# Performance work log

Measured on AMD Instinct MI355X. Metric: run time of the kernel, lower is better.

Reference implementation:

```python
import jax, jax.numpy as jnp
import numpy as np

T, B, D, H = 2048, 2, 1024, 16
DPH = D // H
SCALE = DPH ** -0.5


def setup_inputs() -> dict:
    key = jax.random.key(0)
    ks = jax.random.split(key, 5)
    x = jax.random.normal(ks[0], (T, B, D), dtype=jnp.float32)
    Wk = jax.random.normal(ks[1], (D, D), dtype=jnp.float32) * 0.02
    Wv = jax.random.normal(ks[2], (D, D), dtype=jnp.float32) * 0.02
    Wq = jax.random.normal(ks[3], (D, D), dtype=jnp.float32) * 0.02
    Wo = jax.random.normal(ks[4], (D, D), dtype=jnp.float32) * 0.02
    # causal mask: True marks positions to hide (masked_fill semantics)
    mask = jnp.triu(jnp.ones((T, T), dtype=bool), k=1)
    return {"x": x, "Wk": Wk, "Wv": Wv, "Wq": Wq, "Wo": Wo, "mask": mask}


def _split_heads(y):
    # 't b (d h) -> b h t d' : d_per_head is the OUTER factor of the split
    t, b, _ = y.shape
    return y.reshape(t, b, DPH, H).transpose(1, 3, 0, 2)  # [b, h, t, d]


def reference(x, Wk, Wv, Wq, Wo, mask):
    # nn.Linear(bias=False): y = x @ W.T
    k = _split_heads(x @ Wk.T)
    v = _split_heads(x @ Wv.T)
    q = _split_heads(x @ Wq.T)
    scores = jnp.einsum('bhid,bhjd->bhij', q, k) * SCALE  # [b,h,t,t]
    scores = jnp.where(mask, -jnp.inf, scores)
    attn = jax.nn.softmax(scores, axis=-1)
    # dropout is identity in eval mode
    out = jnp.einsum('bhij,bhjd->bhid', attn, v)  # [b,h,t,d]
    # 'b h t d -> t b (h d)' : heads are the OUTER factor of the merge
    out = out.transpose(2, 0, 1, 3).reshape(x.shape[0], x.shape[1], D)
    return out @ Wo.T
```

## Files before the change

kernel.cpp:

```cpp
#include <hip/hip_runtime.h>

#define T_LEN   2048
#define BATCH   2
#define DMODEL  1024
#define NHEAD   16
#define DHEAD   64
#define MROWS   4096
#define KDIM    1024
#define NDIM    1024
#define ATT_SC2 (0.125f * 1.44269504088896f)

typedef unsigned short u16;
typedef unsigned int   u32;
typedef u16   u16x8 __attribute__((ext_vector_type(8)));
typedef u16   u16x4 __attribute__((ext_vector_type(4)));
typedef __bf16 bf16x8 __attribute__((ext_vector_type(8)));
typedef float f32x4 __attribute__((ext_vector_type(4)));

__device__ __forceinline__ u16 f2bf(float f) {
  u32 u = __builtin_bit_cast(u32, f);
  u += 0x7fffu + ((u >> 16) & 1u);
  return (u16)(u >> 16);
}

__device__ __forceinline__ u16 bfc(float f) {
  return __builtin_bit_cast(u16, (__bf16)f);
}

__device__ __forceinline__ f32x4 mfma16(u16x8 a, u16x8 b, f32x4 c) {
  return __builtin_amdgcn_mfma_f32_16x16x32_bf16(
      __builtin_bit_cast(bf16x8, a), __builtin_bit_cast(bf16x8, b), c, 0, 0, 0);
}

__device__ __forceinline__ void gload16(const u16* g, u16* l) {
  __builtin_amdgcn_global_load_lds((const __attribute__((address_space(1))) void*)g,
                                   (__attribute__((address_space(3))) void*)l,
                                   16, 0, 0);
}

#define XN 4194304u
__global__ __launch_bounds__(256) void cast_all(
    const float* __restrict__ x,  const float* __restrict__ wk,
    const float* __restrict__ wv, const float* __restrict__ wq,
    const float* __restrict__ wo, u16* __restrict__ ws) {
  size_t i = ((size_t)blockIdx.x * 256 + threadIdx.x) * 4;
  const float* src; size_t soff, doff; float sc = 1.0f;
  if (i < XN) {
    int m = (int)(i >> 10), d = (int)(i & 1023);
    int t = m >> 1, b = m & 1;
    src = x; soff = i;
    doff = ((size_t)(b * 2048 + t) << 10) + d;
  } else {
    size_t off = i - XN;
    int wi = (int)(off >> 20);
    off &= 1048575u;
    int u = (int)(off >> 10), c = (int)(off & 1023);
    src = (wi == 0) ? wk : (wi == 1) ? wv : (wi == 2) ? wq : wo;
    soff = off;
    if (wi == 3) {
      doff = XN + 3u * 1048576u + off;
    } else {
      int slot = (wi == 2) ? 0 : (wi == 0) ? 1 : 2;
      int up = (u & 15) * 64 + (u >> 4);
      doff = XN + (size_t)slot * 1048576u + ((size_t)up << 10) + c;
      if (wi == 2) sc = ATT_SC2;
    }
  }
  float4 v = *reinterpret_cast<const float4*>(src + soff);
  u16x4 o;
  o.s0 = f2bf(v.x * sc); o.s1 = f2bf(v.y * sc); o.s2 = f2bf(v.z * sc); o.s3 = f2bf(v.w * sc);
  *reinterpret_cast<u16x4*>(ws + doff) = o;
}

__global__ __launch_bounds__(256, 2) void gemm_qkv(
    const u16* __restrict__ xbm, const u16* __restrict__ Wqkv,
    u16* __restrict__ Qh, u16* __restrict__ Kh, u16* __restrict__ Vt) {
  __shared__ __align__(16) u16 As[256 * 64];
  __shared__ __align__(16) u16 Bs[128 * 64];

  const int tid = threadIdx.x;
  const int l  = tid & 63, w = tid >> 6;
  const int lr = l & 15,  lg = l >> 4;
  const int wm = w >> 1,  wn = w & 1;

  const int blk  = blockIdx.x;
  const int wgid = (blk & 7) * 48 + (blk >> 3);

  const u16 *A, *W;
  int m0, n0, isV;
  if (wgid < 256) {
    const int bx = wgid >> 4, by = wgid & 15;
    A = xbm; W = Wqkv; m0 = by * 256; n0 = bx * 128; isV = 0;
  } else {
    const int v = wgid - 256;
    const int vby = v >> 5, vbx = v & 31;
    A = Wqkv + (2048u << 10); W = xbm; m0 = vby * 256; n0 = vbx * 128; isV = 1;
  }

  f32x4 acc[8][4];
#pragma unroll
  for (int i = 0; i < 8; ++i)
#pragma unroll
    for (int j = 0; j < 4; ++j) acc[i][j] = (f32x4)(0.0f);

  for (int k0 = 0; k0 < KDIM; k0 += 64) {
#pragma unroll
    for (int i = 0; i < 8; ++i) {
      const int base = i * 256 + w * 64;
      const int p = base + l;
      const int r = p >> 3, c = p & 7;
      gload16(A + (size_t)(m0 + r) * KDIM + k0 + ((c ^ (r & 7)) << 3),
              As + (size_t)base * 8);
    }
#pragma unroll
    for (int i = 0; i < 4; ++i) {
      const int base = i * 256 + w * 64;
      const int p = base + l;
      const int r = p >> 3, c = p & 7;
      gload16(W + (size_t)(n0 + r) * KDIM + k0 + ((c ^ (r & 7)) << 3),
              Bs + (size_t)base * 8);
    }
    __syncthreads();

#pragma unroll
    for (int ks = 0; ks < 2; ++ks) {
      const int cr = ks * 4 + lg;
      u16x8 bf_[4];
#pragma unroll
      for (int ni = 0; ni < 4; ++ni) {
        const int rr = wn * 64 + ni * 16 + lr;
        bf_[ni] = *reinterpret_cast<const u16x8*>(Bs + rr * 64 + ((cr ^ (rr & 7)) << 3));
      }
      __builtin_amdgcn_s_setprio(1);
#pragma unroll
      for (int mi = 0; mi < 8; ++mi) {
        const int rr = wm * 128 + mi * 16 + lr;
        const u16x8 af = *reinterpret_cast<const u16x8*>(
            As + rr * 64 + ((cr ^ (rr & 7)) << 3));
#pragma unroll
        for (int ni = 0; ni < 4; ++ni)
          acc[mi][ni] = mfma16(af, bf_[ni], acc[mi][ni]);
      }
      __builtin_amdgcn_s_setprio(0);
    }
    __syncthreads();
  }

#pragma unroll
  for (int mi = 0; mi < 8; ++mi)
#pragma unroll
    for (int ni = 0; ni < 4; ++ni)
#pragma unroll
      for (int r = 0; r < 4; ++r) {
        const int row = m0 + wm * 128 + mi * 16 + lg * 4 + r;
        const int col = n0 + wn * 64 + ni * 16 + lr;
        const u16 v = bfc(acc[mi][ni][r]);
        if (!isV) {
          const int bb = row >> 11, t = row & 2047;
          const int c = col & 1023, hh = c >> 6, dp = c & 63;
          u16* d = (col < 1024) ? Qh : Kh;
          d[(((size_t)(bb * NHEAD + hh) << 11) + t) * 64 + dp] = v;
        } else {
          const int hh = row >> 6, dp = row & 63;
          const int bb = col >> 11, t = col & 2047;
          Vt[((((size_t)(bb * NHEAD + hh)) * 64 + dp) << 11) + t] = v;
        }
      }
}

__global__ __launch_bounds__(256) void gemm_o(
    const u16* __restrict__ A, const u16* __restrict__ W, float* __restrict__ out) {
  __shared__ __align__(16) u16 As[128 * 64];
  __shared__ __align__(16) u16 Bs[64 * 64];

  const int tid = threadIdx.x;
  const int l  = tid & 63, w = tid >> 6;
  const int lr = l & 15,  lg = l >> 4;
  const int wm = w >> 1,  wn = w & 1;

  const int blk  = blockIdx.x;
  const int wgid = (blk & 7) * 64 + (blk >> 3);
  const int bx = wgid >> 5, by = wgid & 31;
  const int m0 = by * 128;
  const int n0 = bx * 64;

  f32x4 acc[4][2];
#pragma unroll
  for (int i = 0; i < 4; ++i)
#pragma unroll
    for (int j = 0; j < 2; ++j) acc[i][j] = (f32x4)(0.0f);

  for (int k0 = 0; k0 < KDIM; k0 += 64) {
#pragma unroll
    for (int i = 0; i < 4; ++i) {
      const int base = i * 256 + w * 64;
      const int p = base + l;
      const int r = p >> 3, c = p & 7;
      gload16(A + (size_t)(m0 + r) * KDIM + k0 + ((c ^ (r & 7)) << 3),
              As + (size_t)base * 8);
    }
#pragma unroll
    for (int i = 0; i < 2; ++i) {
      const int base = i * 256 + w * 64;
      const int p = base + l;
      const int r = p >> 3, c = p & 7;
      gload16(W + (size_t)(n0 + r) * KDIM + k0 + ((c ^ (r & 7)) << 3),
              Bs + (size_t)base * 8);
    }
    __syncthreads();

#pragma unroll
    for (int ks = 0; ks < 2; ++ks) {
      const int cr = ks * 4 + lg;
      u16x8 bf_[2];
#pragma unroll
      for (int ni = 0; ni < 2; ++ni) {
        const int rr = wn * 32 + ni * 16 + lr;
        bf_[ni] = *reinterpret_cast<const u16x8*>(Bs + rr * 64 + ((cr ^ (rr & 7)) << 3));
      }
      __builtin_amdgcn_s_setprio(1);
#pragma unroll
      for (int mi = 0; mi < 4; ++mi) {
        const int rr = wm * 64 + mi * 16 + lr;
        const u16x8 af = *reinterpret_cast<const u16x8*>(
            As + rr * 64 + ((cr ^ (rr & 7)) << 3));
#pragma unroll
        for (int ni = 0; ni < 2; ++ni)
          acc[mi][ni] = mfma16(af, bf_[ni], acc[mi][ni]);
      }
      __builtin_amdgcn_s_setprio(0);
    }
    __syncthreads();
  }

#pragma unroll
  for (int mi = 0; mi < 4; ++mi)
#pragma unroll
    for (int ni = 0; ni < 2; ++ni)
#pragma unroll
      for (int r = 0; r < 4; ++r) {
        const int row = m0 + wm * 64 + mi * 16 + lg * 4 + r;
        const int col = n0 + wn * 32 + ni * 16 + lr;
        const int t = row & 2047, bb = row >> 11;
        out[((size_t)(t * 2 + bb) << 10) + col] = acc[mi][ni][r];
      }
}

__global__ __launch_bounds__(256, 2) void attn_fwd(
    const u16* __restrict__ Qh, const u16* __restrict__ Kh,
    const u16* __restrict__ Vt, u16* __restrict__ Aout) {
  __shared__ __align__(16) u16 smem[36864];

  const int tid = threadIdx.x;
  const int l = tid & 63, w = tid >> 6;
  const int lr = l & 15, lg = l >> 4;
  const int wk = w & 1, wq = w >> 1;
  const int blk = blockIdx.x;
  const int bxx = (blk >> 3) & 15;
  const int bh  = ((blk >> 7) << 3) + (blk & 7);
  const int b = bh >> 4, h = bh & 15;

  const u16* kg = Kh + ((size_t)bh << 17);
  const u16* vg = Vt + ((size_t)bh << 17);
  u16* Pw = smem + 32768 + w * 1024;

  float* redO = reinterpret_cast<float*>(smem);
  float* redS = reinterpret_cast<float*>(smem + 32768);

  const u16x8 ones = {0x3F80,0x3F80,0x3F80,0x3F80,0x3F80,0x3F80,0x3F80,0x3F80};

  auto stage = [&](int buf, int kv0) {
    u16* kb = smem + buf * 8192;
    u16* vb = smem + 16384 + buf * 8192;
#pragma unroll
    for (int j = 0; j < 4; ++j) {
      const int base = (j * 4 + w) * 64;
      const int gg = base + l;
      const int rk = gg >> 3, ck = gg & 7;
      gload16(kg + (size_t)(kv0 + rk) * 64 + ((ck ^ (rk & 7)) << 3),
              kb + (size_t)base * 8);
      const int rv = gg >> 4, cv = gg & 15;
      gload16(vg + ((size_t)rv << 11) + kv0 + ((cv ^ (rv & 15)) << 3),
              vb + (size_t)base * 8);
    }
  };

  for (int ph = 0; ph < 2; ++ph) {
    const int qb = ph ? bxx : 31 - bxx;
    const int qbw = qb * 64 + wq * 32;

    u16x8 qf[2][2];
#pragma unroll
    for (int g = 0; g < 2; ++g) {
      const int qrow = qbw + g * 16 + lr;
      const u16* qptr = Qh + (((size_t)bh << 11) + qrow) * 64 + lg * 8;
      qf[g][0] = *reinterpret_cast<const u16x8*>(qptr);
      qf[g][1] = *reinterpret_cast<const u16x8*>(qptr + 32);
    }

    f32x4 oacc[2][4];
#pragma unroll
    for (int g = 0; g < 2; ++g)
#pragma unroll
      for (int i = 0; i < 4; ++i) oacc[g][i] = (f32x4)(0.0f);
    f32x4 sum4[2] = {(f32x4)(0.0f), (f32x4)(0.0f)};

    const int npair = (qb + 2) >> 1;
    stage(0, 0);
    __syncthreads();

    int cur = 0;
    for (int t = 0; t < npair; ++t) {
      const int kv0 = t * 128;
      if (t + 1 < npair) stage(cur ^ 1, kv0 + 128);

      const int kvw = kv0 + wk * 64;
      if (kvw <= qbw + 31) {
        const u16* kb = smem + cur * 8192;
        const u16* vb = smem + 16384 + cur * 8192;

        u16x8 kf[4][2];
#pragma unroll
        for (int tt = 0; tt < 4; ++tt) {
          const int row = wk * 64 + tt * 16 + lr;
          kf[tt][0] = *reinterpret_cast<const u16x8*>(
              kb + row * 64 + ((lg ^ (row & 7)) << 3));
          kf[tt][1] = *reinterpret_cast<const u16x8*>(
              kb + row * 64 + (((4 + lg) ^ (row & 7)) << 3));
        }
        u16x8 vf[2][4];
#pragma unroll
        for (int kh = 0; kh < 2; ++kh)
#pragma unroll
          for (int ni = 0; ni < 4; ++ni) {
            const int dr = ni * 16 + lr;
            const int ck = wk * 8 + kh * 4 + lg;
            vf[kh][ni] = *reinterpret_cast<const u16x8*>(
                vb + dr * 128 + ((ck ^ (dr & 15)) << 3));
          }

#pragma unroll
        for (int g = 0; g < 2; ++g) {
          const int qbg = qbw + g * 16;
          if (kvw <= qbg + 15) {
            const bool diag = (kvw + 63 > qbg);
            const int qrow = qbg + lr;

            __builtin_amdgcn_s_setprio(1);
#pragma unroll
            for (int tt = 0; tt < 4; ++tt) {
              f32x4 sacc = (f32x4)(0.0f);
              sacc = mfma16(kf[tt][0], qf[g][0], sacc);
              sacc = mfma16(kf[tt][1], qf[g][1], sacc);
              u16x4 pk;
#pragma unroll
              for (int r = 0; r < 4; ++r) {
                const int kv = kvw + tt * 16 + lg * 4 + r;
                const float s = (diag && kv > qrow) ? -1e30f : sacc[r];
                pk[r] = bfc(__builtin_amdgcn_exp2f(s - 8.0f));
              }
              *reinterpret_cast<u16x4*>(
                  &Pw[lr * 64 + (((tt * 2 + (lg >> 1)) ^ (lr & 7)) << 3)
                      + ((lg & 1) << 2)]) = pk;
            }

#pragma unroll
            for (int kh = 0; kh < 2; ++kh) {
              const u16x8 pa = *reinterpret_cast<const u16x8*>(
                  &Pw[lr * 64 + (((kh * 4 + lg) ^ (lr & 7)) << 3)]);
              sum4[g] = mfma16(pa, ones, sum4[g]);
#pragma unroll
              for (int ni = 0; ni < 4; ++ni)
                oacc[g][ni] = mfma16(pa, vf[kh][ni], oacc[g][ni]);
            }
            __builtin_amdgcn_s_setprio(0);
          }
        }
      }

      __syncthreads();
      cur ^= 1;
    }

    if (wk) {
      float* po = redO + wq * 2176;
#pragma unroll
      for (int g = 0; g < 2; ++g) {
#pragma unroll
        for (int ni = 0; ni < 4; ++ni)
#pragma unroll
          for (int r = 0; r < 4; ++r)
            po[(g * 16 + lg * 4 + r) * 68 + ni * 16 + lr] = oacc[g][ni][r];
        if (lr == 0) {
#pragma unroll
          for (int r = 0; r < 4; ++r)
            redS[wq * 32 + g * 16 + lg * 4 + r] = sum4[g][r];
        }
      }
    }
    __syncthreads();

    if (!wk) {
      const float* po = redO + wq * 2176;
#pragma unroll
      for (int g = 0; g < 2; ++g) {
        f32x4 ss = sum4[g];
#pragma unroll
        for (int r = 0; r < 4; ++r)
          ss[r] += redS[wq * 32 + g * 16 + lg * 4 + r];
#pragma unroll
        for (int r = 0; r < 4; ++r) {
          const float inv = 1.0f / ss[r];
          const int q = qbw + g * 16 + lg * 4 + r;
          const size_t rowbase = (((size_t)(b * 2048 + q)) << 10) + h * DHEAD;
#pragma unroll
          for (int ni = 0; ni < 4; ++ni)
            Aout[rowbase + ni * 16 + lr] = bfc(
                (oacc[g][ni][r] + po[(g * 16 + lg * 4 + r) * 68 + ni * 16 + lr])
                * inv);
        }
      }
    }
    __syncthreads();
  }
}

extern "C" void kernel_launch(void* const* d_in, const int* in_sizes, int n_in,
                              void* d_out, int out_size, void* d_ws, size_t ws_size,
                              hipStream_t stream) {
  const float* x  = (const float*)d_in[0];
  const float* Wk = (const float*)d_in[1];
  const float* Wv = (const float*)d_in[2];
  const float* Wq = (const float*)d_in[3];
  const float* Wo = (const float*)d_in[4];

  u16* ws   = (u16*)d_ws;
  u16* xbm  = ws;
  u16* Wqkv = xbm + 4194304;
  u16* Wob  = Wqkv + 3145728;
  u16* Qh   = Wob + 1048576;
  u16* Kh   = Qh  + 4194304;
  u16* Vt   = Kh  + 4194304;
  u16* Aout = Vt  + 4194304;

  cast_all<<<8192, 256, 0, stream>>>(x, Wk, Wv, Wq, Wo, ws);

  gemm_qkv<<<384, 256, 0, stream>>>(xbm, Wqkv, Qh, Kh, Vt);

  attn_fwd<<<512, 256, 0, stream>>>(Qh, Kh, Vt, Aout);

  gemm_o<<<512, 256, 0, stream>>>(Aout, Wob, (float*)d_out);
}
```

Measured before the change: 107.1 us.

## Process both causal-balanced query blocks in one shared KV sweep

The attention kernel previously handled two query blocks (31-bxx and bxx) one after another, streaming K/V tiles from global memory twice. It now loads Q fragments for both blocks up front and makes a single pass over the KV range of the longer block, applying each staged K/V tile to both query blocks. This removes the duplicate K/V staging and one set of pipeline start-ups and barriers. The cost is twice the accumulator and Q registers per thread, which under launch_bounds(256,2) may cause spills or lower occupancy, and the reduction area in shared memory doubles.

After: 110.1 us. 2.8% more time.

```diff
diff --git a/kernel.cpp b/kernel.cpp
--- a/kernel.cpp
+++ b/kernel.cpp
@@ -260,6 +260,8 @@
   const int bh  = ((blk >> 7) << 3) + (blk & 7);
   const int b = bh >> 4, h = bh & 15;
 
+  const int qb_[2] = {31 - bxx, bxx};
+
   const u16* kg = Kh + ((size_t)bh << 17);
   const u16* vg = Vt + ((size_t)bh << 17);
   u16* Pw = smem + 32768 + w * 1024;
@@ -285,60 +287,64 @@
     }
   };
 
-  for (int ph = 0; ph < 2; ++ph) {
-    const int qb = ph ? bxx : 31 - bxx;
-    const int qbw = qb * 64 + wq * 32;
-
-    u16x8 qf[2][2];
+  u16x8 qf[2][2][2];
+#pragma unroll
+  for (int qs = 0; qs < 2; ++qs)
 #pragma unroll
     for (int g = 0; g < 2; ++g) {
-      const int qrow = qbw + g * 16 + lr;
+      const int qrow = qb_[qs] * 64 + wq * 32 + g * 16 + lr;
       const u16* qptr = Qh + (((size_t)bh << 11) + qrow) * 64 + lg * 8;
-      qf[g][0] = *reinterpret_cast<const u16x8*>(qptr);
-      qf[g][1] = *reinterpret_cast<const u16x8*>(qptr + 32);
-    }
-
-    f32x4 oacc[2][4];
+      qf[qs][g][0] = *reinterpret_cast<const u16x8*>(qptr);
+      qf[qs][g][1] = *reinterpret_cast<const u16x8*>(qptr + 32);
+    }
+
+  f32x4 oacc[2][2][4];
+#pragma unroll
+  for (int qs = 0; qs < 2; ++qs)
 #pragma unroll
     for (int g = 0; g < 2; ++g)
 #pragma unroll
-      for (int i = 0; i < 4; ++i) oacc[g][i] = (f32x4)(0.0f);
-    f32x4 sum4[2] = {(f32x4)(0.0f), (f32x4)(0.0f)};
-
-    const int npair = (qb + 2) >> 1;
-    stage(0, 0);
-    __syncthreads();
-
-    int cur = 0;
-    for (int t = 0; t < npair; ++t) {
-      const int kv0 = t * 128;
-      if (t + 1 < npair) stage(cur ^ 1, kv0 + 128);
-
-      const int kvw = kv0 + wk * 64;
-      if (kvw <= qbw + 31) {
-        const u16* kb = smem + cur * 8192;
-        const u16* vb = smem + 16384 + cur * 8192;
-
-        u16x8 kf[4][2];
-#pragma unroll
-        for (int tt = 0; tt < 4; ++tt) {
-          const int row = wk * 64 + tt * 16 + lr;
-          kf[tt][0] = *reinterpret_cast<const u16x8*>(
-              kb + row * 64 + ((lg ^ (row & 7)) << 3));
-          kf[tt][1] = *reinterpret_cast<const u16x8*>(
-              kb + row * 64 + (((4 + lg) ^ (row & 7)) << 3));
+      for (int i = 0; i < 4; ++i) oacc[qs][g][i] = (f32x4)(0.0f);
+  f32x4 sum4[2][2] = {{(f32x4)(0.0f), (f32x4)(0.0f)},
+                      {(f32x4)(0.0f), (f32x4)(0.0f)}};
+
+  const int npair = (qb_[0] + 2) >> 1;
+  stage(0, 0);
+  __syncthreads();
+
+  int cur = 0;
+  for (int t = 0; t < npair; ++t) {
+    const int kv0 = t * 128;
+    if (t + 1 < npair) stage(cur ^ 1, kv0 + 128);
+
+    const int kvw = kv0 + wk * 64;
+    if (kvw <= qb_[0] * 64 + wq * 32 + 31) {
+      const u16* kb = smem + cur * 8192;
+      const u16* vb = smem + 16384 + cur * 8192;
+
+      u16x8 kf[4][2];
+#pragma unroll
+      for (int tt = 0; tt < 4; ++tt) {
+        const int row = wk * 64 + tt * 16 + lr;
+        kf[tt][0] = *reinterpret_cast<const u16x8*>(
+            kb + row * 64 + ((lg ^ (row & 7)) << 3));
+        kf[tt][1] = *reinterpret_cast<const u16x8*>(
+            kb + row * 64 + (((4 + lg) ^ (row & 7)) << 3));
+      }
+      u16x8 vf[2][4];
+#pragma unroll
+      for (int kh = 0; kh < 2; ++kh)
+#pragma unroll
+        for (int ni = 0; ni < 4; ++ni) {
+          const int dr = ni * 16 + lr;
+          const int ck = wk * 8 + kh * 4 + lg;
+          vf[kh][ni] = *reinterpret_cast<const u16x8*>(
+              vb + dr * 128 + ((ck ^ (dr & 15)) << 3));
         }
-        u16x8 vf[2][4];
-#pragma unroll
-        for (int kh = 0; kh < 2; ++kh)
-#pragma unroll
-          for (int ni = 0; ni < 4; ++ni) {
-            const int dr = ni * 16 + lr;
-            const int ck = wk * 8 + kh * 4 + lg;
-            vf[kh][ni] = *reinterpret_cast<const u16x8*>(
-                vb + dr * 128 + ((ck ^ (dr & 15)) << 3));
-          }
-
+
+#pragma unroll
+      for (int qs = 0; qs < 2; ++qs) {
+        const int qbw = qb_[qs] * 64 + wq * 32;
 #pragma unroll
         for (int g = 0; g < 2; ++g) {
           const int qbg = qbw + g * 16;
@@ -350,8 +356,8 @@
 #pragma unroll
             for (int tt = 0; tt < 4; ++tt) {
               f32x4 sacc = (f32x4)(0.0f);
-              sacc = mfma16(kf[tt][0], qf[g][0], sacc);
-              sacc = mfma16(kf[tt][1], qf[g][1], sacc);
+              sacc = mfma16(kf[tt][0], qf[qs][g][0], sacc);
+              sacc = mfma16(kf[tt][1], qf[qs][g][1], sacc);
               u16x4 pk;
 #pragma unroll
               for (int r = 0; r < 4; ++r) {
@@ -368,46 +374,53 @@
             for (int kh = 0; kh < 2; ++kh) {
               const u16x8 pa = *reinterpret_cast<const u16x8*>(
                   &Pw[lr * 64 + (((kh * 4 + lg) ^ (lr & 7)) << 3)]);
-              sum4[g] = mfma16(pa, ones, sum4[g]);
+              sum4[qs][g] = mfma16(pa, ones, sum4[qs][g]);
 #pragma unroll
               for (int ni = 0; ni < 4; ++ni)
-                oacc[g][ni] = mfma16(pa, vf[kh][ni], oacc[g][ni]);
+                oacc[qs][g][ni] = mfma16(pa, vf[kh][ni], oacc[qs][g][ni]);
             }
             __builtin_amdgcn_s_setprio(0);
           }
         }
       }
-
-      __syncthreads();
-      cur ^= 1;
-    }
-
-    if (wk) {
-      float* po = redO + wq * 2176;
+    }
+
+    __syncthreads();
+    cur ^= 1;
+  }
+
+  if (wk) {
+#pragma unroll
+    for (int qs = 0; qs < 2; ++qs) {
+      float* po = redO + (qs * 2 + wq) * 2176;
 #pragma unroll
       for (int g = 0; g < 2; ++g) {
 #pragma unroll
         for (int ni = 0; ni < 4; ++ni)
 #pragma unroll
           for (int r = 0; r < 4; ++r)
-            po[(g * 16 + lg * 4 + r) * 68 + ni * 16 + lr] = oacc[g][ni][r];
+            po[(g * 16 + lg * 4 + r) * 68 + ni * 16 + lr] = oacc[qs][g][ni][r];
         if (lr == 0) {
 #pragma unroll
           for (int r = 0; r < 4; ++r)
-            redS[wq * 32 + g * 16 + lg * 4 + r] = sum4[g][r];
+            redS[qs * 64 + wq * 32 + g * 16 + lg * 4 + r] = sum4[qs][g][r];
         }
       }
     }
-    __syncthreads();
-
-    if (!wk) {
-      const float* po = redO + wq * 2176;
+  }
+  __syncthreads();
+
+  if (!wk) {
+#pragma unroll
+    for (int qs = 0; qs < 2; ++qs) {
+      const float* po = redO + (qs * 2 + wq) * 2176;
+      const int qbw = qb_[qs] * 64 + wq * 32;
 #pragma unroll
       for (int g = 0; g < 2; ++g) {
-        f32x4 ss = sum4[g];
+        f32x4 ss = sum4[qs][g];
 #pragma unroll
         for (int r = 0; r < 4; ++r)
-          ss[r] += redS[wq * 32 + g * 16 + lg * 4 + r];
+          ss[r] += redS[qs * 64 + wq * 32 + g * 16 + lg * 4 + r];
 #pragma unroll
         for (int r = 0; r < 4; ++r) {
           const float inv = 1.0f / ss[r];
@@ -416,12 +429,11 @@
 #pragma unroll
           for (int ni = 0; ni < 4; ++ni)
             Aout[rowbase + ni * 16 + lr] = bfc(
-                (oacc[g][ni][r] + po[(g * 16 + lg * 4 + r) * 68 + ni * 16 + lr])
-                * inv);
+                (oacc[qs][g][ni][r]
+                 + po[(g * 16 + lg * 4 + r) * 68 + ni * 16 + lr]) * inv);
         }
       }
     }
-    __syncthreads();
   }
 }
 
```

## Fuse x fp32-to-bf16 cast into QKV GEMM tile loads

Applied to the files above, without the earlier changes.

Removes the standalone cast of x to bf16 in the cast kernel, which now converts only the weights. The QKV GEMM reads fp32 x directly, converts it in registers and writes the swizzled bf16 tile to LDS, remapping rows from the (t,b) order to batch-major. This drops a 16 MB read/write round-trip and halves the cast grid. In exchange, x loads become synchronous register loads instead of async global-to-LDS loads, and each x tile is re-read and re-converted by many workgroups, doubling the bytes moved per x tile.

After: 137.9 us. 28.8% more time.

```diff
diff --git a/kernel.cpp b/kernel.cpp
--- a/kernel.cpp
+++ b/kernel.cpp
@@ -38,42 +38,32 @@
                                    16, 0, 0);
 }
 
-#define XN 4194304u
-__global__ __launch_bounds__(256) void cast_all(
-    const float* __restrict__ x,  const float* __restrict__ wk,
-    const float* __restrict__ wv, const float* __restrict__ wq,
-    const float* __restrict__ wo, u16* __restrict__ ws) {
+__global__ __launch_bounds__(256) void cast_w(
+    const float* __restrict__ wk, const float* __restrict__ wv,
+    const float* __restrict__ wq, const float* __restrict__ wo,
+    u16* __restrict__ ws) {
   size_t i = ((size_t)blockIdx.x * 256 + threadIdx.x) * 4;
-  const float* src; size_t soff, doff; float sc = 1.0f;
-  if (i < XN) {
-    int m = (int)(i >> 10), d = (int)(i & 1023);
-    int t = m >> 1, b = m & 1;
-    src = x; soff = i;
-    doff = ((size_t)(b * 2048 + t) << 10) + d;
+  const int wi = (int)(i >> 20);
+  const size_t off = i & 1048575u;
+  const float* src = (wi == 0) ? wk : (wi == 1) ? wv : (wi == 2) ? wq : wo;
+  const float sc = (wi == 2) ? ATT_SC2 : 1.0f;
+  size_t doff;
+  if (wi == 3) {
+    doff = 3u * 1048576u + off;
   } else {
-    size_t off = i - XN;
-    int wi = (int)(off >> 20);
-    off &= 1048575u;
-    int u = (int)(off >> 10), c = (int)(off & 1023);
-    src = (wi == 0) ? wk : (wi == 1) ? wv : (wi == 2) ? wq : wo;
-    soff = off;
-    if (wi == 3) {
-      doff = XN + 3u * 1048576u + off;
-    } else {
-      int slot = (wi == 2) ? 0 : (wi == 0) ? 1 : 2;
-      int up = (u & 15) * 64 + (u >> 4);
-      doff = XN + (size_t)slot * 1048576u + ((size_t)up << 10) + c;
-      if (wi == 2) sc = ATT_SC2;
-    }
+    const int u = (int)(off >> 10), c = (int)(off & 1023);
+    const int slot = (wi == 2) ? 0 : (wi == 0) ? 1 : 2;
+    const int up = (u & 15) * 64 + (u >> 4);
+    doff = (size_t)slot * 1048576u + ((size_t)up << 10) + c;
   }
-  float4 v = *reinterpret_cast<const float4*>(src + soff);
+  float4 v = *reinterpret_cast<const float4*>(src + off);
   u16x4 o;
   o.s0 = f2bf(v.x * sc); o.s1 = f2bf(v.y * sc); o.s2 = f2bf(v.z * sc); o.s3 = f2bf(v.w * sc);
   *reinterpret_cast<u16x4*>(ws + doff) = o;
 }
 
 __global__ __launch_bounds__(256, 2) void gemm_qkv(
-    const u16* __restrict__ xbm, const u16* __restrict__ Wqkv,
+    const float* __restrict__ xf, const u16* __restrict__ Wqkv,
     u16* __restrict__ Qh, u16* __restrict__ Kh, u16* __restrict__ Vt) {
   __shared__ __align__(16) u16 As[256 * 64];
   __shared__ __align__(16) u16 Bs[128 * 64];
@@ -86,16 +76,16 @@
   const int blk  = blockIdx.x;
   const int wgid = (blk & 7) * 48 + (blk >> 3);
 
-  const u16 *A, *W;
   int m0, n0, isV;
   if (wgid < 256) {
     const int bx = wgid >> 4, by = wgid & 15;
-    A = xbm; W = Wqkv; m0 = by * 256; n0 = bx * 128; isV = 0;
+    m0 = by * 256; n0 = bx * 128; isV = 0;
   } else {
     const int v = wgid - 256;
     const int vby = v >> 5, vbx = v & 31;
-    A = Wqkv + (2048u << 10); W = xbm; m0 = vby * 256; n0 = vbx * 128; isV = 1;
+    m0 = vby * 256; n0 = vbx * 128; isV = 1;
   }
+  const u16* Wv = Wqkv + (2048u << 10);
 
   f32x4 acc[8][4];
 #pragma unroll
@@ -104,21 +94,52 @@
     for (int j = 0; j < 4; ++j) acc[i][j] = (f32x4)(0.0f);
 
   for (int k0 = 0; k0 < KDIM; k0 += 64) {
-#pragma unroll
-    for (int i = 0; i < 8; ++i) {
-      const int base = i * 256 + w * 64;
-      const int p = base + l;
-      const int r = p >> 3, c = p & 7;
-      gload16(A + (size_t)(m0 + r) * KDIM + k0 + ((c ^ (r & 7)) << 3),
-              As + (size_t)base * 8);
-    }
-#pragma unroll
-    for (int i = 0; i < 4; ++i) {
-      const int base = i * 256 + w * 64;
-      const int p = base + l;
-      const int r = p >> 3, c = p & 7;
-      gload16(W + (size_t)(n0 + r) * KDIM + k0 + ((c ^ (r & 7)) << 3),
-              Bs + (size_t)base * 8);
+    if (!isV) {
+#pragma unroll
+      for (int i = 0; i < 4; ++i) {
+        const int base = i * 256 + w * 64;
+        const int p = base + l;
+        const int r = p >> 3, c = p & 7;
+        gload16(Wqkv + (size_t)(n0 + r) * KDIM + k0 + ((c ^ (r & 7)) << 3),
+                Bs + (size_t)base * 8);
+      }
+#pragma unroll
+      for (int i = 0; i < 8; ++i) {
+        const int p = i * 256 + w * 64 + l;
+        const int r = p >> 3, c = p & 7;
+        const int m = m0 + r;
+        const int xrow = ((m & 2047) << 1) + (m >> 11);
+        const float* sp = xf + ((size_t)xrow << 10) + k0 + ((c ^ (r & 7)) << 3);
+        const float4 v0 = *reinterpret_cast<const float4*>(sp);
+        const float4 v1 = *reinterpret_cast<const float4*>(sp + 4);
+        u16x8 o;
+        o[0] = bfc(v0.x); o[1] = bfc(v0.y); o[2] = bfc(v0.z); o[3] = bfc(v0.w);
+        o[4] = bfc(v1.x); o[5] = bfc(v1.y); o[6] = bfc(v1.z); o[7] = bfc(v1.w);
+        *reinterpret_cast<u16x8*>(As + (size_t)p * 8) = o;
+      }
+    } else {
+#pragma unroll
+      for (int i = 0; i < 8; ++i) {
+        const int base = i * 256 + w * 64;
+        const int p = base + l;
+        const int r = p >> 3, c = p & 7;
+        gload16(Wv + (size_t)(m0 + r) * KDIM + k0 + ((c ^ (r & 7)) << 3),
+                As + (size_t)base * 8);
+      }
+#pragma unroll
+      for (int i = 0; i < 4; ++i) {
+        const int p = i * 256 + w * 64 + l;
+        const int r = p >> 3, c = p & 7;
+        const int n = n0 + r;
+        const int xrow = ((n & 2047) << 1) + (n >> 11);
+        const float* sp = xf + ((size_t)xrow << 10) + k0 + ((c ^ (r & 7)) << 3);
+        const float4 v0 = *reinterpret_cast<const float4*>(sp);
+        const float4 v1 = *reinterpret_cast<const float4*>(sp + 4);
+        u16x8 o;
+        o[0] = bfc(v0.x); o[1] = bfc(v0.y); o[2] = bfc(v0.z); o[3] = bfc(v0.w);
+        o[4] = bfc(v1.x); o[5] = bfc(v1.y); o[6] = bfc(v1.z); o[7] = bfc(v1.w);
+        *reinterpret_cast<u16x8*>(Bs + (size_t)p * 8) = o;
+      }
     }
     __syncthreads();
 
@@ -435,17 +456,16 @@
   const float* Wo = (const float*)d_in[4];
 
   u16* ws   = (u16*)d_ws;
-  u16* xbm  = ws;
-  u16* Wqkv = xbm + 4194304;
+  u16* Wqkv = ws;
   u16* Wob  = Wqkv + 3145728;
   u16* Qh   = Wob + 1048576;
   u16* Kh   = Qh  + 4194304;
   u16* Vt   = Kh  + 4194304;
   u16* Aout = Vt  + 4194304;
 
-  cast_all<<<8192, 256, 0, stream>>>(x, Wk, Wv, Wq, Wo, ws);
-
-  gemm_qkv<<<384, 256, 0, stream>>>(xbm, Wqkv, Qh, Kh, Vt);
+  cast_w<<<4096, 256, 0, stream>>>(Wk, Wv, Wq, Wo, ws);
+
+  gemm_qkv<<<384, 256, 0, stream>>>(x, Wqkv, Qh, Kh, Vt);
 
   attn_fwd<<<512, 256, 0, stream>>>(Qh, Kh, Vt, Aout);
 
```
